# Optimization experiments

Hardware: AMD Instinct MI355X
Metric: run time of the kernel (lower is better)

The kernel has to match this reference:

```python
import jax, jax.numpy as jnp
import numpy as np

B, T, N, D, K, MP = 32, 50, 50000, 128, 16, 50
HID = (D + K) // 2  # WP_1 out features


def _normalize(x, axis=-1, eps=1e-12):
    return x / jnp.maximum(jnp.linalg.norm(x, axis=axis, keepdims=True), eps)


def _layer_norm(x, g, b, eps=1e-6):
    m = jnp.mean(x, axis=-1, keepdims=True)
    v = jnp.var(x, axis=-1, keepdims=True)
    return (x - m) * jax.lax.rsqrt(v + eps) * g + b


def setup_inputs() -> dict:
    key = jax.random.key(0)
    ks = jax.random.split(key, 20)
    std = 0.01
    session = jax.random.randint(ks[0], (B, T), 1, N + 1)  # ids >= 1, no padding
    lengths = jnp.full((B,), T, dtype=jnp.int32)
    isValidSession = jnp.ones((B * T,), dtype=bool)
    inp = {
        'session': session,
        'lengths': lengths,
        'tau': 1,
        'isValidSession': isValidSession,
        'train': 1,
        'I_emb': jax.random.normal(ks[1], (N + 1, D)) * std,
        'P_emb': jax.random.normal(ks[2], (K, D)) * std,
        'E_P_emb': jax.random.normal(ks[3], (MP, D)) * std,
        'E_S_emb': jax.random.normal(ks[4], (MP + 1, D)) * std,
        'V': _normalize(jax.random.normal(ks[5], (K, D))),
        'WP1': jax.random.normal(ks[6], (HID, D)),   # torch Linear weight [out, in]
        'WP2': jax.random.normal(ks[7], (K, HID)),
        'Wq': jax.random.normal(ks[8], (D, D)) / np.sqrt(D),
        'Wk': jax.random.normal(ks[9], (D, D)) / np.sqrt(D),
        'Wv': jax.random.normal(ks[10], (D, D)) / np.sqrt(D),
        'Wo': jax.random.normal(ks[11], (D, D)) / np.sqrt(D),
        'FF1': jax.random.normal(ks[12], (D, D)) / np.sqrt(D),
        'FF2': jax.random.normal(ks[13], (D, D)) / np.sqrt(D),
        'ln1_g': jnp.ones((D,)), 'ln1_b': jnp.zeros((D,)),
        'ln2_g': jnp.ones((D,)), 'ln2_b': jnp.zeros((D,)),
    }
    return inp


def _forward(session, lengths, tau, I_emb, P_emb, E_P_emb, E_S_emb, V,
             WP1, WP2, Wq, Wk, Wv, Wo, FF1, FF2, ln1_g, ln1_b, ln2_g, ln2_b):
    Vn = _normalize(V)                               # forward renormalizes V rows
    lf = lengths.astype(jnp.float32)
    isValidPos = (session != 0).astype(jnp.float32)  # [B,T]
    sess_emb = I_emb[session]                        # [B,T,D]
    EP = E_P_emb[jnp.arange(T) + (MP - T)]           # [T,D]
    es_idx = jnp.maximum(jnp.arange(T)[None, :] + 1 - (T - lengths[:, None]), 0)
    ES = E_S_emb[es_idx]                             # [B,T,D]

    # ---- ProxySelection (dropout in eval mode = identity) ----
    X = isValidPos[..., None] * (sess_emb + EP[None])
    X = jax.nn.leaky_relu(X @ WP1.T, 0.1) @ WP2.T    # [B,T,K]
    fP = jnp.sum(X, axis=1) / lf[:, None]
    pi = jax.nn.softmax(fP / tau, axis=-1)           # [B,K]
    p_s = pi @ P_emb                                 # [B,D]
    v = _normalize(pi @ Vn)                          # [B,D]

    # ---- SIE: single-layer self-attention encoder ----
    Xs = sess_emb + ES
    subseq = jnp.triu(jnp.ones((T, T), dtype=bool), 1)[None]        # causal
    pad = (session == 0)[:, None, :]                                # key padding
    mask = (subseq | pad)
    mask = mask.at[:, :, 0].set(False)
    non_pad = (session != 0).astype(jnp.float32)[..., None]
    q, kk, vv = Xs @ Wq.T, Xs @ Wk.T, Xs @ Wv.T
    scores = jnp.einsum('btd,bsd->bts', q, kk) / np.sqrt(D)
    scores = jnp.where(mask, -1e9, scores)
    attn = jax.nn.softmax(scores, axis=-1)
    h = (attn @ vv) @ Wo.T
    h = _layer_norm(h + Xs, ln1_g, ln1_b) * non_pad
    f = jax.nn.relu(h @ FF1.T) @ FF2.T
    s_s = _layer_norm(f + h, ln2_g, ln2_b) * non_pad                # [B,T,D]

    # project out v component per sample
    s_s_proj = s_s - v[:, None, :] * jnp.sum(v[:, None, :] * s_s, axis=-1, keepdims=True)
    orthogonal = jnp.abs(jnp.sum(v * p_s, axis=-1)) / jnp.linalg.norm(p_s, axis=-1)

    # ---- train_phase: dist(p_s+s_s_proj[b,t], I_proj_b) for all items ----
    # I_proj_b = I - v_b (v_b . I); with ||v_b||=1:
    #   ||F - I_proj||^2 = ||F||^2 - 2(F.I - (F.v)(v.I)) + ||I||^2 - (v.I)^2
    F = p_s[:, None, :] + s_s_proj                   # [B,T,D]
    vI = jnp.einsum('nd,bd->bn', I_emb, v)           # [B,N+1]
    Fv = jnp.einsum('btd,bd->bt', F, v)              # [B,T]
    FI = jnp.einsum('btd,nd->btn', F, I_emb)         # [B,T,N+1]
    Fn2 = jnp.sum(F * F, axis=-1)                    # [B,T]
    In2 = jnp.sum(I_emb * I_emb, axis=-1)[None, :] - vI * vI  # [B,N+1]
    dist = Fn2[..., None] - 2.0 * (FI - Fv[..., None] * vI[:, None, :]) + In2[:, None, :]
    return dist.reshape(B * T, N + 1), orthogonal


def reference(session, lengths, tau, isValidSession, train,
              I_emb, P_emb, E_P_emb, E_S_emb, V,
              WP1, WP2, Wq, Wk, Wv, Wo, FF1, FF2, ln1_g, ln1_b, ln2_g, ln2_b):
    # isValidSession is all-True and train=1: distance rows = all (b,t) pairs
    return _forward(session, lengths, tau, I_emb, P_emb, E_P_emb, E_S_emb, V,
                    WP1, WP2, Wq, Wk, Wv, Wo, FF1, FF2, ln1_g, ln1_b, ln2_g, ln2_b)
```

## Files before the change

kernel.cpp:

```cpp
#include <hip/hip_runtime.h>
#include <math.h>

#define B   32
#define T   50
#define N1  50001
#define D   128
#define KP  16
#define MP  50
#define HID 72
#define BT  (B*T)

typedef __attribute__((ext_vector_type(8))) short short8v;
typedef __attribute__((ext_vector_type(4))) float f32x4;

__device__ __forceinline__ unsigned short f2bf(float x) {
    unsigned u = __float_as_uint(x);
    u += 0x7fffu + ((u >> 16) & 1u);
    return (unsigned short)(u >> 16);
}

__device__ __forceinline__ float blockReduceSum128(float val, volatile float* sbuf) {
    for (int off = 32; off > 0; off >>= 1) val += __shfl_down(val, off, 64);
    __syncthreads();
    if ((threadIdx.x & 63) == 0) sbuf[threadIdx.x >> 6] = val;
    __syncthreads();
    return sbuf[0] + sbuf[1];
}

__global__ void k_proxy_x2(const int* __restrict__ session,
                           const float* __restrict__ I_emb,
                           const float* __restrict__ EP_emb,
                           const float* __restrict__ WP1,
                           const float* __restrict__ WP2,
                           float* __restrict__ X2) {
    int bt = blockIdx.x; int t = bt % T;
    int tid = threadIdx.x;
    __shared__ __align__(16) float x[D];
    __shared__ float h[HID];
    int sid = session[bt];
    float val = 0.f;
    if (sid != 0) val = I_emb[(size_t)sid * D + tid] + EP_emb[(t + MP - T) * D + tid];
    x[tid] = val;
    __syncthreads();
    if (tid < HID) {
        float acc = 0.f;
        const float4* w4 = (const float4*)(WP1 + tid * D);
        const float4* x4 = (const float4*)x;
        #pragma unroll 8
        for (int k = 0; k < D / 4; ++k) {
            float4 w = w4[k]; float4 xv = x4[k];
            acc += xv.x * w.x + xv.y * w.y + xv.z * w.z + xv.w * w.w;
        }
        h[tid] = acc > 0.f ? acc : 0.1f * acc;
    }
    __syncthreads();
    if (tid < KP) {
        float acc = 0.f;
        const float* w = WP2 + tid * HID;
        for (int k = 0; k < HID; ++k) acc += h[k] * w[k];
        X2[bt * KP + tid] = acc;
    }
}

__global__ void k_proxy_head(const float* __restrict__ X2,
                             const int* __restrict__ lengths,
                             const int* __restrict__ tau_i,
                             const float* __restrict__ P_emb,
                             const float* __restrict__ V,
                             float* __restrict__ ps_o,
                             float* __restrict__ v_o,
                             float* __restrict__ orth_o) {
    int b = blockIdx.x; int tid = threadIdx.x;
    __shared__ float pi[KP];
    __shared__ float vn[KP];
    __shared__ float sbuf[2];
    float tau = (float)tau_i[0];
    float lf = (float)lengths[b];
    if (tid < KP) {
        float s = 0.f;
        for (int t = 0; t < T; ++t) s += X2[(b * T + t) * KP + tid];
        pi[tid] = (s / lf) / tau;
    }
    if (tid < KP) {
        float s = 0.f;
        for (int d = 0; d < D; ++d) { float z = V[tid * D + d]; s += z * z; }
        vn[tid] = fmaxf(sqrtf(s), 1e-12f);
    }
    __syncthreads();
    if (tid == 0) {
        float m = pi[0];
        for (int k = 1; k < KP; ++k) m = fmaxf(m, pi[k]);
        float s = 0.f;
        for (int k = 0; k < KP; ++k) { float e = expf(pi[k] - m); pi[k] = e; s += e; }
        for (int k = 0; k < KP; ++k) pi[k] /= s;
    }
    __syncthreads();
    float p = 0.f, vt = 0.f;
    for (int k = 0; k < KP; ++k) {
        p  += pi[k] * P_emb[k * D + tid];
        vt += pi[k] * (V[k * D + tid] / vn[k]);
    }
    float vsq = blockReduceSum128(vt * vt, sbuf);
    float vv = vt / fmaxf(sqrtf(vsq), 1e-12f);
    float psq = blockReduceSum128(p * p, sbuf);
    float dvp = blockReduceSum128(vv * p, sbuf);
    ps_o[b * D + tid] = p;
    v_o[b * D + tid] = vv;
    if (tid == 0) orth_o[b] = fabsf(dvp) / sqrtf(psq);
}

__global__ void k_xs_qkv(const int* __restrict__ session,
                         const int* __restrict__ lengths,
                         const float* __restrict__ I_emb,
                         const float* __restrict__ ES_emb,
                         const float* __restrict__ Wq,
                         const float* __restrict__ Wk,
                         const float* __restrict__ Wv,
                         float* __restrict__ xs_o, float* __restrict__ q_o,
                         float* __restrict__ k_o, float* __restrict__ v_o) {
    int bt = blockIdx.x; int b = bt / T; int t = bt % T;
    int tid = threadIdx.x;
    __shared__ __align__(16) float xs[D];
    int sid = session[bt];
    int es = t + 1 - (T - lengths[b]); if (es < 0) es = 0;
    float x = I_emb[(size_t)sid * D + tid] + ES_emb[es * D + tid];
    xs[tid] = x;
    __syncthreads();
    float aq = 0.f, ak = 0.f, av = 0.f;
    const float4* wq4 = (const float4*)(Wq + tid * D);
    const float4* wk4 = (const float4*)(Wk + tid * D);
    const float4* wv4 = (const float4*)(Wv + tid * D);
    const float4* x4  = (const float4*)xs;
    #pragma unroll 8
    for (int k = 0; k < D / 4; ++k) {
        float4 xv = x4[k];
        float4 a = wq4[k], bq = wk4[k], c = wv4[k];
        aq += xv.x * a.x + xv.y * a.y + xv.z * a.z + xv.w * a.w;
        ak += xv.x * bq.x + xv.y * bq.y + xv.z * bq.z + xv.w * bq.w;
        av += xv.x * c.x + xv.y * c.y + xv.z * c.z + xv.w * c.w;
    }
    xs_o[bt * D + tid] = x; q_o[bt * D + tid] = aq; k_o[bt * D + tid] = ak; v_o[bt * D + tid] = av;
}

__global__ void k_attn(const int* __restrict__ session,
                       const float* __restrict__ q,
                       const float* __restrict__ kk,
                       const float* __restrict__ vv,
                       float* __restrict__ ho) {
    int bt = blockIdx.x; int b = bt / T; int t = bt % T;
    int tid = threadIdx.x;
    __shared__ __align__(16) float qs[D];
    __shared__ float attn[64];
    qs[tid] = q[bt * D + tid];
    __syncthreads();
    if (tid < T) {
        int s = tid;
        bool allowed = (s == 0) || ((s <= t) && (session[b * T + s] != 0));
        float sc = -1e9f;
        if (allowed) {
            float a = 0.f;
            const float4* kr = (const float4*)(kk + (size_t)(b * T + s) * D);
            const float4* q4 = (const float4*)qs;
            #pragma unroll 8
            for (int d = 0; d < D / 4; ++d) {
                float4 kv = kr[d]; float4 qv = q4[d];
                a += qv.x * kv.x + qv.y * kv.y + qv.z * kv.z + qv.w * kv.w;
            }
            sc = a * 0.088388347648318447f;
        }
        attn[s] = sc;
    }
    __syncthreads();
    if (tid < 64) {
        float vsc = (tid < T) ? attn[tid] : -1e30f;
        float m = vsc;
        for (int off = 32; off > 0; off >>= 1) m = fmaxf(m, __shfl_xor(m, off, 64));
        float e = (tid < T) ? expf(vsc - m) : 0.f;
        float ssum = e;
        for (int off = 32; off > 0; off >>= 1) ssum += __shfl_xor(ssum, off, 64);
        if (tid < T) attn[tid] = e / ssum;
    }
    __syncthreads();
    float acc = 0.f;
    for (int s = 0; s < T; ++s) acc += attn[s] * vv[(size_t)(b * T + s) * D + tid];
    ho[bt * D + tid] = acc;
}

__global__ void k_post_attn(const int* __restrict__ session,
                            const float* __restrict__ ho,
                            const float* __restrict__ Wo,
                            const float* __restrict__ xs,
                            const float* __restrict__ g1, const float* __restrict__ b1,
                            float* __restrict__ h_o) {
    int bt = blockIdx.x; int tid = threadIdx.x;
    __shared__ __align__(16) float hr[D];
    __shared__ float sbuf[2];
    hr[tid] = ho[bt * D + tid];
    __syncthreads();
    float a = 0.f;
    const float4* w4 = (const float4*)(Wo + tid * D);
    const float4* h4 = (const float4*)hr;
    #pragma unroll 8
    for (int k = 0; k < D / 4; ++k) {
        float4 w = w4[k]; float4 hv = h4[k];
        a += hv.x * w.x + hv.y * w.y + hv.z * w.z + hv.w * w.w;
    }
    float x = a + xs[bt * D + tid];
    float mean = blockReduceSum128(x, sbuf) * (1.f / D);
    float dx = x - mean;
    float var = blockReduceSum128(dx * dx, sbuf) * (1.f / D);
    float y = dx * rsqrtf(var + 1e-6f) * g1[tid] + b1[tid];
    h_o[bt * D + tid] = y * ((session[bt] != 0) ? 1.f : 0.f);
}

__global__ void k_ffn_G(const int* __restrict__ session,
                        const float* __restrict__ h,
                        const float* __restrict__ FF1, const float* __restrict__ FF2,
                        const float* __restrict__ g2, const float* __restrict__ b2,
                        const float* __restrict__ ps, const float* __restrict__ v,
                        short* __restrict__ G16, float* __restrict__ Fn2) {
    int bt = blockIdx.x; int b = bt / T; int tid = threadIdx.x;
    __shared__ __align__(16) float hr[D];
    __shared__ __align__(16) float t1[D];
    __shared__ float sbuf[2];
    float hx = h[bt * D + tid];
    hr[tid] = hx;
    __syncthreads();
    float a = 0.f;
    const float4* w14 = (const float4*)(FF1 + tid * D);
    const float4* h4 = (const float4*)hr;
    #pragma unroll 8
    for (int k = 0; k < D / 4; ++k) {
        float4 w = w14[k]; float4 hv = h4[k];
        a += hv.x * w.x + hv.y * w.y + hv.z * w.z + hv.w * w.w;
    }
    t1[tid] = fmaxf(a, 0.f);
    __syncthreads();
    float f = 0.f;
    const float4* w24 = (const float4*)(FF2 + tid * D);
    const float4* t4 = (const float4*)t1;
    #pragma unroll 8
    for (int k = 0; k < D / 4; ++k) {
        float4 w = w24[k]; float4 tv = t4[k];
        f += tv.x * w.x + tv.y * w.y + tv.z * w.z + tv.w * w.w;
    }
    float x = f + hx;
    float mean = blockReduceSum128(x, sbuf) * (1.f / D);
    float dx = x - mean;
    float var = blockReduceSum128(dx * dx, sbuf) * (1.f / D);
    float ss = dx * rsqrtf(var + 1e-6f) * g2[tid] + b2[tid];
    ss *= (session[bt] != 0) ? 1.f : 0.f;
    float vb = v[b * D + tid];
    float vs = blockReduceSum128(vb * ss, sbuf);
    float ssp = ss - vb * vs;
    float Fd = ps[b * D + tid] + ssp;
    float Fv = blockReduceSum128(Fd * vb, sbuf);
    float Gd = Fd - Fv * vb;
    float fn2 = blockReduceSum128(Fd * Fd, sbuf);
    G16[bt * D + tid] = (short)f2bf(Gd);
    if (tid == 0) Fn2[bt] = fn2;
}

#define LDK 136

__global__ __launch_bounds__(256) void k_item_mfma(const float* __restrict__ I,
                                                   const float* __restrict__ v,
                                                   float* __restrict__ In2pb) {
    __shared__ __align__(16) short Is[64][LDK];
    __shared__ __align__(16) short Vs[32][LDK];
    __shared__ float sq[64][4];
    __shared__ float in2[64];
    int n0 = blockIdx.x * 64;
    int tid = threadIdx.x;
    {
        int vr = tid >> 3;
        int vc = (tid & 7) * 16;
        const float4* src = (const float4*)&v[vr * D + vc];
        #pragma unroll
        for (int s = 0; s < 4; ++s) {
            float4 f = src[s];
            ushort4 u;
            u.x = f2bf(f.x); u.y = f2bf(f.y); u.z = f2bf(f.z); u.w = f2bf(f.w);
            *(ushort4*)&Vs[vr][vc + s * 4] = u;
        }
    }
    {
        int r = tid >> 2;
        int q = tid & 3;
        int n = n0 + r;
        float ss = 0.f;
        if (n < N1) {
            const float4* src = (const float4*)&I[(size_t)n * D + q * 32];
            #pragma unroll
            for (int s = 0; s < 8; ++s) {
                float4 f = src[s];
                ss += f.x * f.x + f.y * f.y + f.z * f.z + f.w * f.w;
                ushort4 u;
                u.x = f2bf(f.x); u.y = f2bf(f.y); u.z = f2bf(f.z); u.w = f2bf(f.w);
                *(ushort4*)&Is[r][q * 32 + s * 4] = u;
            }
        } else {
            #pragma unroll
            for (int s = 0; s < 8; ++s)
                *(ushort4*)&Is[r][q * 32 + s * 4] = make_ushort4(0, 0, 0, 0);
        }
        sq[r][q] = ss;
    }
    __syncthreads();
    if (tid < 64) in2[tid] = sq[tid][0] + sq[tid][1] + sq[tid][2] + sq[tid][3];
    __syncthreads();
    int w = tid >> 6, l = tid & 63, lr = l & 15, lg = l >> 4;
    f32x4 acc[2] = {{0.f,0.f,0.f,0.f},{0.f,0.f,0.f,0.f}};
    short8v af[4];
    #pragma unroll
    for (int ks = 0; ks < 4; ++ks)
        af[ks] = *(const short8v*)&Is[w * 16 + lr][ks * 32 + lg * 8];
    #pragma unroll
    for (int nt = 0; nt < 2; ++nt) {
        #pragma unroll
        for (int ks = 0; ks < 4; ++ks) {
            short8v bf = *(const short8v*)&Vs[nt * 16 + lr][ks * 32 + lg * 8];
            acc[nt] = __builtin_amdgcn_mfma_f32_16x16x32_bf16(af[ks], bf, acc[nt], 0, 0, 0);
        }
    }
    #pragma unroll
    for (int nt = 0; nt < 2; ++nt) {
        int b = nt * 16 + lr;
        #pragma unroll
        for (int i = 0; i < 4; ++i) {
            int item = w * 16 + lg * 4 + i;
            int n = n0 + item;
            if (n < N1) {
                float dvi = acc[nt][i];
                In2pb[(size_t)b * N1 + n] = in2[item] - dvi * dvi;
            }
        }
    }
}

__global__ __launch_bounds__(256) void k_dist_mfma(const short* __restrict__ G16,
                                                   const float* __restrict__ I,
                                                   const float* __restrict__ Fn2,
                                                   const float* __restrict__ In2pb,
                                                   float* __restrict__ out) {
    __shared__ __align__(16) short As[64][LDK];
    __shared__ __align__(16) short Bs[64][LDK];
    int bt0 = blockIdx.y * 64;
    int n0  = blockIdx.x * 64;
    int tid = threadIdx.x;
    int r = tid >> 4;
    int c = (tid & 15) * 8;
    #pragma unroll
    for (int s = 0; s < 4; ++s) {
        int row = r + s * 16;
        *(short8v*)&As[row][c] = *(const short8v*)&G16[(size_t)(bt0 + row) * D + c];
    }
    {
        int br = tid >> 2;
        int bq = (tid & 3) * 32;
        int n = n0 + br;
        if (n < N1) {
            const float4* src = (const float4*)&I[(size_t)n * D + bq];
            #pragma unroll
            for (int s = 0; s < 8; ++s) {
                float4 f = src[s];
                ushort4 u;
                u.x = f2bf(f.x); u.y = f2bf(f.y); u.z = f2bf(f.z); u.w = f2bf(f.w);
                *(ushort4*)&Bs[br][bq + s * 4] = u;
            }
        } else {
            #pragma unroll
            for (int s = 0; s < 8; ++s)
                *(ushort4*)&Bs[br][bq + s * 4] = make_ushort4(0, 0, 0, 0);
        }
    }
    __syncthreads();
    int w  = tid >> 6;
    int l  = tid & 63;
    int lr = l & 15;
    int lg = l >> 4;
    f32x4 acc[4] = {{0.f,0.f,0.f,0.f},{0.f,0.f,0.f,0.f},{0.f,0.f,0.f,0.f},{0.f,0.f,0.f,0.f}};
    short8v af[4];
    #pragma unroll
    for (int ks = 0; ks < 4; ++ks)
        af[ks] = *(const short8v*)&As[w * 16 + lr][ks * 32 + lg * 8];
    #pragma unroll
    for (int nt = 0; nt < 4; ++nt) {
        #pragma unroll
        for (int ks = 0; ks < 4; ++ks) {
            short8v bf = *(const short8v*)&Bs[nt * 16 + lr][ks * 32 + lg * 8];
            acc[nt] = __builtin_amdgcn_mfma_f32_16x16x32_bf16(af[ks], bf, acc[nt], 0, 0, 0);
        }
    }
    #pragma unroll
    for (int nt = 0; nt < 4; ++nt) {
        int col = n0 + nt * 16 + lr;
        if (col < N1) {
            #pragma unroll
            for (int i = 0; i < 4; ++i) {
                int row = bt0 + w * 16 + lg * 4 + i;
                int b = row / T;
                out[(size_t)row * N1 + col] = Fn2[row] + In2pb[(size_t)b * N1 + col] - 2.f * acc[nt][i];
            }
        }
    }
}

extern "C" void kernel_launch(void* const* d_in, const int* in_sizes, int n_in,
                              void* d_out, int out_size, void* d_ws, size_t ws_size,
                              hipStream_t stream) {
    const int*   session = (const int*)d_in[0];
    const int*   lengths = (const int*)d_in[1];
    const int*   tau     = (const int*)d_in[2];
    const float* I_emb   = (const float*)d_in[5];
    const float* P_emb   = (const float*)d_in[6];
    const float* EP      = (const float*)d_in[7];
    const float* ES      = (const float*)d_in[8];
    const float* V       = (const float*)d_in[9];
    const float* WP1     = (const float*)d_in[10];
    const float* WP2     = (const float*)d_in[11];
    const float* Wq      = (const float*)d_in[12];
    const float* Wk      = (const float*)d_in[13];
    const float* Wv      = (const float*)d_in[14];
    const float* Wo      = (const float*)d_in[15];
    const float* FF1     = (const float*)d_in[16];
    const float* FF2     = (const float*)d_in[17];
    const float* g1      = (const float*)d_in[18];
    const float* b1      = (const float*)d_in[19];
    const float* g2      = (const float*)d_in[20];
    const float* b2      = (const float*)d_in[21];
    float* out = (float*)d_out;
    float* ws  = (float*)d_ws;

    float* wsX2   = ws;
    float* wsPs   = wsX2 + 25600;
    float* wsV    = wsPs + 4096;
    float* wsXs   = wsV + 4096;
    float* wsQ    = wsXs + 204800;
    float* wsK    = wsQ + 204800;
    float* wsVv   = wsK + 204800;
    float* wsHo   = wsVv + 204800;
    float* wsH    = wsHo + 204800;
    float* wsFn2  = wsH + 204800;
    float* wsIn2  = wsFn2 + 1600;
    short* wsG16  = (short*)(wsIn2 + 1600032);

    float* orth_out = out + (size_t)BT * N1;

    k_proxy_x2 <<<BT, 128, 0, stream>>>(session, I_emb, EP, WP1, WP2, wsX2);
    k_proxy_head<<<B, 128, 0, stream>>>(wsX2, lengths, tau, P_emb, V, wsPs, wsV, orth_out);
    k_xs_qkv  <<<BT, 128, 0, stream>>>(session, lengths, I_emb, ES, Wq, Wk, Wv,
                                       wsXs, wsQ, wsK, wsVv);
    k_attn    <<<BT, 128, 0, stream>>>(session, wsQ, wsK, wsVv, wsHo);
    k_post_attn<<<BT, 128, 0, stream>>>(session, wsHo, Wo, wsXs, g1, b1, wsH);
    k_ffn_G   <<<BT, 128, 0, stream>>>(session, wsH, FF1, FF2, g2, b2, wsPs, wsV,
                                       wsG16, wsFn2);
    k_item_mfma<<<(N1 + 63) / 64, 256, 0, stream>>>(I_emb, wsV, wsIn2);
    dim3 gdist((N1 + 63) / 64, BT / 64);
    k_dist_mfma<<<gdist, 256, 0, stream>>>(wsG16, I_emb, wsFn2, wsIn2, out);
}
```

Before: 308.3 us.

## Fuse front-end kernels, cache bf16 item table, enlarge distance GEMM tile

Merges the proxy and QKV kernels into one, and merges attention, post-attention layernorm and the FFN into one kernel, which removes launches and intermediate global round trips. The item-norm kernel now also writes a bf16 copy of the item embeddings. The distance kernel reads that copy instead of re-converting fp32 rows in every block, and each block now covers 128 session rows, so item tiles are reloaded fewer times. The cost is extra workspace and an extra bf16 write pass over the item table, plus higher register and LDS use per distance block.

```diff
diff --git a/kernel.cpp b/kernel.cpp
--- a/kernel.cpp
+++ b/kernel.cpp
@@ -27,21 +27,47 @@
     return sbuf[0] + sbuf[1];
 }
 
-__global__ void k_proxy_x2(const int* __restrict__ session,
-                           const float* __restrict__ I_emb,
-                           const float* __restrict__ EP_emb,
-                           const float* __restrict__ WP1,
-                           const float* __restrict__ WP2,
-                           float* __restrict__ X2) {
-    int bt = blockIdx.x; int t = bt % T;
+__global__ void k_fused_emb(const int* __restrict__ session,
+                            const int* __restrict__ lengths,
+                            const float* __restrict__ I_emb,
+                            const float* __restrict__ EP_emb,
+                            const float* __restrict__ ES_emb,
+                            const float* __restrict__ WP1,
+                            const float* __restrict__ WP2,
+                            const float* __restrict__ Wq,
+                            const float* __restrict__ Wk,
+                            const float* __restrict__ Wv,
+                            float* __restrict__ X2,
+                            float* __restrict__ xs_o, float* __restrict__ q_o,
+                            float* __restrict__ k_o, float* __restrict__ v_o) {
+    int bt = blockIdx.x; int b = bt / T; int t = bt % T;
     int tid = threadIdx.x;
     __shared__ __align__(16) float x[D];
+    __shared__ __align__(16) float xs[D];
     __shared__ float h[HID];
     int sid = session[bt];
-    float val = 0.f;
-    if (sid != 0) val = I_emb[(size_t)sid * D + tid] + EP_emb[(t + MP - T) * D + tid];
-    x[tid] = val;
-    __syncthreads();
+    float ie = I_emb[(size_t)sid * D + tid];
+    float xv_ = (sid != 0) ? (ie + EP_emb[(t + MP - T) * D + tid]) : 0.f;
+    int es = t + 1 - (T - lengths[b]); if (es < 0) es = 0;
+    float xsv = ie + ES_emb[es * D + tid];
+    x[tid] = xv_;
+    xs[tid] = xsv;
+    __syncthreads();
+    float aq = 0.f, ak = 0.f, av = 0.f;
+    {
+        const float4* wq4 = (const float4*)(Wq + tid * D);
+        const float4* wk4 = (const float4*)(Wk + tid * D);
+        const float4* wv4 = (const float4*)(Wv + tid * D);
+        const float4* x4  = (const float4*)xs;
+        #pragma unroll 8
+        for (int k = 0; k < D / 4; ++k) {
+            float4 xv = x4[k];
+            float4 a = wq4[k], bq = wk4[k], c = wv4[k];
+            aq += xv.x * a.x + xv.y * a.y + xv.z * a.z + xv.w * a.w;
+            ak += xv.x * bq.x + xv.y * bq.y + xv.z * bq.z + xv.w * bq.w;
+            av += xv.x * c.x + xv.y * c.y + xv.z * c.z + xv.w * c.w;
+        }
+    }
     if (tid < HID) {
         float acc = 0.f;
         const float4* w4 = (const float4*)(WP1 + tid * D);
@@ -53,6 +79,8 @@
         }
         h[tid] = acc > 0.f ? acc : 0.1f * acc;
     }
+    xs_o[bt * D + tid] = xsv;
+    q_o[bt * D + tid] = aq; k_o[bt * D + tid] = ak; v_o[bt * D + tid] = av;
     __syncthreads();
     if (tid < KP) {
         float acc = 0.f;
@@ -109,48 +137,24 @@
     if (tid == 0) orth_o[b] = fabsf(dvp) / sqrtf(psq);
 }
 
-__global__ void k_xs_qkv(const int* __restrict__ session,
-                         const int* __restrict__ lengths,
-                         const float* __restrict__ I_emb,
-                         const float* __restrict__ ES_emb,
-                         const float* __restrict__ Wq,
-                         const float* __restrict__ Wk,
-                         const float* __restrict__ Wv,
-                         float* __restrict__ xs_o, float* __restrict__ q_o,
-                         float* __restrict__ k_o, float* __restrict__ v_o) {
-    int bt = blockIdx.x; int b = bt / T; int t = bt % T;
-    int tid = threadIdx.x;
-    __shared__ __align__(16) float xs[D];
-    int sid = session[bt];
-    int es = t + 1 - (T - lengths[b]); if (es < 0) es = 0;
-    float x = I_emb[(size_t)sid * D + tid] + ES_emb[es * D + tid];
-    xs[tid] = x;
-    __syncthreads();
-    float aq = 0.f, ak = 0.f, av = 0.f;
-    const float4* wq4 = (const float4*)(Wq + tid * D);
-    const float4* wk4 = (const float4*)(Wk + tid * D);
-    const float4* wv4 = (const float4*)(Wv + tid * D);
-    const float4* x4  = (const float4*)xs;
-    #pragma unroll 8
-    for (int k = 0; k < D / 4; ++k) {
-        float4 xv = x4[k];
-        float4 a = wq4[k], bq = wk4[k], c = wv4[k];
-        aq += xv.x * a.x + xv.y * a.y + xv.z * a.z + xv.w * a.w;
-        ak += xv.x * bq.x + xv.y * bq.y + xv.z * bq.z + xv.w * bq.w;
-        av += xv.x * c.x + xv.y * c.y + xv.z * c.z + xv.w * c.w;
-    }
-    xs_o[bt * D + tid] = x; q_o[bt * D + tid] = aq; k_o[bt * D + tid] = ak; v_o[bt * D + tid] = av;
-}
-
-__global__ void k_attn(const int* __restrict__ session,
-                       const float* __restrict__ q,
-                       const float* __restrict__ kk,
-                       const float* __restrict__ vv,
-                       float* __restrict__ ho) {
+__global__ void k_fused_attn(const int* __restrict__ session,
+                             const float* __restrict__ q,
+                             const float* __restrict__ kk,
+                             const float* __restrict__ vv,
+                             const float* __restrict__ xs,
+                             const float* __restrict__ Wo,
+                             const float* __restrict__ g1, const float* __restrict__ b1,
+                             const float* __restrict__ FF1, const float* __restrict__ FF2,
+                             const float* __restrict__ g2, const float* __restrict__ b2,
+                             const float* __restrict__ ps, const float* __restrict__ v,
+                             short* __restrict__ G16, float* __restrict__ Fn2) {
     int bt = blockIdx.x; int b = bt / T; int t = bt % T;
     int tid = threadIdx.x;
     __shared__ __align__(16) float qs[D];
+    __shared__ __align__(16) float buf1[D];
+    __shared__ __align__(16) float buf2[D];
     __shared__ float attn[64];
+    __shared__ float sbuf[2];
     qs[tid] = q[bt * D + tid];
     __syncthreads();
     if (tid < T) {
@@ -183,72 +187,53 @@
     __syncthreads();
     float acc = 0.f;
     for (int s = 0; s < T; ++s) acc += attn[s] * vv[(size_t)(b * T + s) * D + tid];
-    ho[bt * D + tid] = acc;
-}
-
-__global__ void k_post_attn(const int* __restrict__ session,
-                            const float* __restrict__ ho,
-                            const float* __restrict__ Wo,
-                            const float* __restrict__ xs,
-                            const float* __restrict__ g1, const float* __restrict__ b1,
-                            float* __restrict__ h_o) {
-    int bt = blockIdx.x; int tid = threadIdx.x;
-    __shared__ __align__(16) float hr[D];
-    __shared__ float sbuf[2];
-    hr[tid] = ho[bt * D + tid];
+    buf1[tid] = acc;
     __syncthreads();
     float a = 0.f;
-    const float4* w4 = (const float4*)(Wo + tid * D);
-    const float4* h4 = (const float4*)hr;
-    #pragma unroll 8
-    for (int k = 0; k < D / 4; ++k) {
-        float4 w = w4[k]; float4 hv = h4[k];
-        a += hv.x * w.x + hv.y * w.y + hv.z * w.z + hv.w * w.w;
-    }
-    float x = a + xs[bt * D + tid];
-    float mean = blockReduceSum128(x, sbuf) * (1.f / D);
-    float dx = x - mean;
+    {
+        const float4* w4 = (const float4*)(Wo + tid * D);
+        const float4* h4 = (const float4*)buf1;
+        #pragma unroll 8
+        for (int k = 0; k < D / 4; ++k) {
+            float4 w = w4[k]; float4 hv = h4[k];
+            a += hv.x * w.x + hv.y * w.y + hv.z * w.z + hv.w * w.w;
+        }
+    }
+    float x1 = a + xs[bt * D + tid];
+    float mean = blockReduceSum128(x1, sbuf) * (1.f / D);
+    float dx = x1 - mean;
     float var = blockReduceSum128(dx * dx, sbuf) * (1.f / D);
-    float y = dx * rsqrtf(var + 1e-6f) * g1[tid] + b1[tid];
-    h_o[bt * D + tid] = y * ((session[bt] != 0) ? 1.f : 0.f);
-}
-
-__global__ void k_ffn_G(const int* __restrict__ session,
-                        const float* __restrict__ h,
-                        const float* __restrict__ FF1, const float* __restrict__ FF2,
-                        const float* __restrict__ g2, const float* __restrict__ b2,
-                        const float* __restrict__ ps, const float* __restrict__ v,
-                        short* __restrict__ G16, float* __restrict__ Fn2) {
-    int bt = blockIdx.x; int b = bt / T; int tid = threadIdx.x;
-    __shared__ __align__(16) float hr[D];
-    __shared__ __align__(16) float t1[D];
-    __shared__ float sbuf[2];
-    float hx = h[bt * D + tid];
-    hr[tid] = hx;
-    __syncthreads();
-    float a = 0.f;
-    const float4* w14 = (const float4*)(FF1 + tid * D);
-    const float4* h4 = (const float4*)hr;
-    #pragma unroll 8
-    for (int k = 0; k < D / 4; ++k) {
-        float4 w = w14[k]; float4 hv = h4[k];
-        a += hv.x * w.x + hv.y * w.y + hv.z * w.z + hv.w * w.w;
-    }
-    t1[tid] = fmaxf(a, 0.f);
+    float hx = (dx * rsqrtf(var + 1e-6f) * g1[tid] + b1[tid]) * ((session[bt] != 0) ? 1.f : 0.f);
+    buf2[tid] = hx;
+    __syncthreads();
+    float a1 = 0.f;
+    {
+        const float4* w4 = (const float4*)(FF1 + tid * D);
+        const float4* h4 = (const float4*)buf2;
+        #pragma unroll 8
+        for (int k = 0; k < D / 4; ++k) {
+            float4 w = w4[k]; float4 hv = h4[k];
+            a1 += hv.x * w.x + hv.y * w.y + hv.z * w.z + hv.w * w.w;
+        }
+    }
+    __syncthreads();
+    buf1[tid] = fmaxf(a1, 0.f);
     __syncthreads();
     float f = 0.f;
-    const float4* w24 = (const float4*)(FF2 + tid * D);
-    const float4* t4 = (const float4*)t1;
-    #pragma unroll 8
-    for (int k = 0; k < D / 4; ++k) {
-        float4 w = w24[k]; float4 tv = t4[k];
-        f += tv.x * w.x + tv.y * w.y + tv.z * w.z + tv.w * w.w;
-    }
-    float x = f + hx;
-    float mean = blockReduceSum128(x, sbuf) * (1.f / D);
-    float dx = x - mean;
-    float var = blockReduceSum128(dx * dx, sbuf) * (1.f / D);
-    float ss = dx * rsqrtf(var + 1e-6f) * g2[tid] + b2[tid];
+    {
+        const float4* w4 = (const float4*)(FF2 + tid * D);
+        const float4* t4 = (const float4*)buf1;
+        #pragma unroll 8
+        for (int k = 0; k < D / 4; ++k) {
+            float4 w = w4[k]; float4 tv = t4[k];
+            f += tv.x * w.x + tv.y * w.y + tv.z * w.z + tv.w * w.w;
+        }
+    }
+    float x2 = f + hx;
+    float mean2 = blockReduceSum128(x2, sbuf) * (1.f / D);
+    float dx2 = x2 - mean2;
+    float var2 = blockReduceSum128(dx2 * dx2, sbuf) * (1.f / D);
+    float ss = dx2 * rsqrtf(var2 + 1e-6f) * g2[tid] + b2[tid];
     ss *= (session[bt] != 0) ? 1.f : 0.f;
     float vb = v[b * D + tid];
     float vs = blockReduceSum128(vb * ss, sbuf);
@@ -265,7 +250,8 @@
 
 __global__ __launch_bounds__(256) void k_item_mfma(const float* __restrict__ I,
                                                    const float* __restrict__ v,
-                                                   float* __restrict__ In2pb) {
+                                                   float* __restrict__ In2pb,
+                                                   unsigned short* __restrict__ I16) {
     __shared__ __align__(16) short Is[64][LDK];
     __shared__ __align__(16) short Vs[32][LDK];
     __shared__ float sq[64][4];
@@ -286,25 +272,26 @@
     }
     {
         int r = tid >> 2;
-        int q = tid & 3;
+        int qq = tid & 3;
         int n = n0 + r;
         float ss = 0.f;
         if (n < N1) {
-            const float4* src = (const float4*)&I[(size_t)n * D + q * 32];
+            const float4* src = (const float4*)&I[(size_t)n * D + qq * 32];
             #pragma unroll
             for (int s = 0; s < 8; ++s) {
                 float4 f = src[s];
                 ss += f.x * f.x + f.y * f.y + f.z * f.z + f.w * f.w;
                 ushort4 u;
                 u.x = f2bf(f.x); u.y = f2bf(f.y); u.z = f2bf(f.z); u.w = f2bf(f.w);
-                *(ushort4*)&Is[r][q * 32 + s * 4] = u;
+                *(ushort4*)&Is[r][qq * 32 + s * 4] = u;
+                *(ushort4*)&I16[(size_t)n * D + qq * 32 + s * 4] = u;
             }
         } else {
             #pragma unroll
             for (int s = 0; s < 8; ++s)
-                *(ushort4*)&Is[r][q * 32 + s * 4] = make_ushort4(0, 0, 0, 0);
-        }
-        sq[r][q] = ss;
+                *(ushort4*)&Is[r][qq * 32 + s * 4] = make_ushort4(0, 0, 0, 0);
+        }
+        sq[r][qq] = ss;
     }
     __syncthreads();
     if (tid < 64) in2[tid] = sq[tid][0] + sq[tid][1] + sq[tid][2] + sq[tid][3];
@@ -339,68 +326,77 @@
 }
 
 __global__ __launch_bounds__(256) void k_dist_mfma(const short* __restrict__ G16,
-                                                   const float* __restrict__ I,
+                                                   const unsigned short* __restrict__ I16,
                                                    const float* __restrict__ Fn2,
                                                    const float* __restrict__ In2pb,
                                                    float* __restrict__ out) {
-    __shared__ __align__(16) short As[64][LDK];
+    __shared__ __align__(16) short As[128][LDK];
     __shared__ __align__(16) short Bs[64][LDK];
-    int bt0 = blockIdx.y * 64;
     int n0  = blockIdx.x * 64;
+    int bt0 = blockIdx.y * 128;
     int tid = threadIdx.x;
     int r = tid >> 4;
     int c = (tid & 15) * 8;
     #pragma unroll
+    for (int s = 0; s < 8; ++s) {
+        int row = r + s * 16;
+        short8v gv = {};
+        if (bt0 + row < BT) gv = *(const short8v*)&G16[(size_t)(bt0 + row) * D + c];
+        *(short8v*)&As[row][c] = gv;
+    }
+    #pragma unroll
     for (int s = 0; s < 4; ++s) {
         int row = r + s * 16;
-        *(short8v*)&As[row][c] = *(const short8v*)&G16[(size_t)(bt0 + row) * D + c];
-    }
-    {
-        int br = tid >> 2;
-        int bq = (tid & 3) * 32;
-        int n = n0 + br;
-        if (n < N1) {
-            const float4* src = (const float4*)&I[(size_t)n * D + bq];
-            #pragma unroll
-            for (int s = 0; s < 8; ++s) {
-                float4 f = src[s];
-                ushort4 u;
-                u.x = f2bf(f.x); u.y = f2bf(f.y); u.z = f2bf(f.z); u.w = f2bf(f.w);
-                *(ushort4*)&Bs[br][bq + s * 4] = u;
-            }
-        } else {
-            #pragma unroll
-            for (int s = 0; s < 8; ++s)
-                *(ushort4*)&Bs[br][bq + s * 4] = make_ushort4(0, 0, 0, 0);
-        }
+        int n = n0 + row;
+        short8v bv = {};
+        if (n < N1) bv = *(const short8v*)&I16[(size_t)n * D + c];
+        *(short8v*)&Bs[row][c] = bv;
     }
     __syncthreads();
     int w  = tid >> 6;
     int l  = tid & 63;
     int lr = l & 15;
     int lg = l >> 4;
-    f32x4 acc[4] = {{0.f,0.f,0.f,0.f},{0.f,0.f,0.f,0.f},{0.f,0.f,0.f,0.f},{0.f,0.f,0.f,0.f}};
-    short8v af[4];
-    #pragma unroll
-    for (int ks = 0; ks < 4; ++ks)
-        af[ks] = *(const short8v*)&As[w * 16 + lr][ks * 32 + lg * 8];
+    short8v af[2][4];
+    #pragma unroll
+    for (int mi = 0; mi < 2; ++mi)
+        #pragma unroll
+        for (int ks = 0; ks < 4; ++ks)
+            af[mi][ks] = *(const short8v*)&As[w * 32 + mi * 16 + lr][ks * 32 + lg * 8];
+    f32x4 acc[2][4];
+    #pragma unroll
+    for (int mi = 0; mi < 2; ++mi)
+        #pragma unroll
+        for (int nt = 0; nt < 4; ++nt) acc[mi][nt] = (f32x4){0.f, 0.f, 0.f, 0.f};
     #pragma unroll
     for (int nt = 0; nt < 4; ++nt) {
-        #pragma unroll
-        for (int ks = 0; ks < 4; ++ks) {
-            short8v bf = *(const short8v*)&Bs[nt * 16 + lr][ks * 32 + lg * 8];
-            acc[nt] = __builtin_amdgcn_mfma_f32_16x16x32_bf16(af[ks], bf, acc[nt], 0, 0, 0);
-        }
-    }
-    #pragma unroll
-    for (int nt = 0; nt < 4; ++nt) {
-        int col = n0 + nt * 16 + lr;
-        if (col < N1) {
+        short8v bf[4];
+        #pragma unroll
+        for (int ks = 0; ks < 4; ++ks)
+            bf[ks] = *(const short8v*)&Bs[nt * 16 + lr][ks * 32 + lg * 8];
+        #pragma unroll
+        for (int mi = 0; mi < 2; ++mi)
+            #pragma unroll
+            for (int ks = 0; ks < 4; ++ks)
+                acc[mi][nt] = __builtin_amdgcn_mfma_f32_16x16x32_bf16(af[mi][ks], bf[ks], acc[mi][nt], 0, 0, 0);
+    }
+    #pragma unroll
+    for (int mi = 0; mi < 2; ++mi) {
+        int rb = bt0 + w * 32 + mi * 16 + lg * 4;
+        if (rb < BT) {
+            float4 fn4 = *(const float4*)&Fn2[rb];
+            float fnv[4] = {fn4.x, fn4.y, fn4.z, fn4.w};
             #pragma unroll
             for (int i = 0; i < 4; ++i) {
-                int row = bt0 + w * 16 + lg * 4 + i;
+                int row = rb + i;
                 int b = row / T;
-                out[(size_t)row * N1 + col] = Fn2[row] + In2pb[(size_t)b * N1 + col] - 2.f * acc[nt][i];
+                const float* inrow = In2pb + (size_t)b * N1;
+                float* orow = out + (size_t)row * N1;
+                #pragma unroll
+                for (int nt = 0; nt < 4; ++nt) {
+                    int col = n0 + nt * 16 + lr;
+                    if (col < N1) orow[col] = fnv[i] + inrow[col] - 2.f * acc[mi][nt][i];
+                }
             }
         }
     }
@@ -439,23 +435,21 @@
     float* wsQ    = wsXs + 204800;
     float* wsK    = wsQ + 204800;
     float* wsVv   = wsK + 204800;
-    float* wsHo   = wsVv + 204800;
-    float* wsH    = wsHo + 204800;
-    float* wsFn2  = wsH + 204800;
+    float* wsFn2  = wsVv + 204800;
     float* wsIn2  = wsFn2 + 1600;
     short* wsG16  = (short*)(wsIn2 + 1600032);
+    unsigned short* wsI16 = (unsigned short*)(wsG16 + 204800);
 
     float* orth_out = out + (size_t)BT * N1;
 
-    k_proxy_x2 <<<BT, 128, 0, stream>>>(session, I_emb, EP, WP1, WP2, wsX2);
+    k_fused_emb <<<BT, 128, 0, stream>>>(session, lengths, I_emb, EP, ES,
+                                         WP1, WP2, Wq, Wk, Wv,
+                                         wsX2, wsXs, wsQ, wsK, wsVv);
     k_proxy_head<<<B, 128, 0, stream>>>(wsX2, lengths, tau, P_emb, V, wsPs, wsV, orth_out);
-    k_xs_qkv  <<<BT, 128, 0, stream>>>(session, lengths, I_emb, ES, Wq, Wk, Wv,
-                                       wsXs, wsQ, wsK, wsVv);
-    k_attn    <<<BT, 128, 0, stream>>>(session, wsQ, wsK, wsVv, wsHo);
-    k_post_attn<<<BT, 128, 0, stream>>>(session, wsHo, Wo, wsXs, g1, b1, wsH);
-    k_ffn_G   <<<BT, 128, 0, stream>>>(session, wsH, FF1, FF2, g2, b2, wsPs, wsV,
-                                       wsG16, wsFn2);
-    k_item_mfma<<<(N1 + 63) / 64, 256, 0, stream>>>(I_emb, wsV, wsIn2);
-    dim3 gdist((N1 + 63) / 64, BT / 64);
-    k_dist_mfma<<<gdist, 256, 0, stream>>>(wsG16, I_emb, wsFn2, wsIn2, out);
-}
+    k_fused_attn<<<BT, 128, 0, stream>>>(session, wsQ, wsK, wsVv, wsXs,
+                                         Wo, g1, b1, FF1, FF2, g2, b2,
+                                         wsPs, wsV, wsG16, wsFn2);
+    k_item_mfma <<<(N1 + 63) / 64, 256, 0, stream>>>(I_emb, wsV, wsIn2, wsI16);
+    dim3 gdist((N1 + 63) / 64, (BT + 127) / 128);
+    k_dist_mfma <<<gdist, 256, 0, stream>>>(wsG16, wsI16, wsFn2, wsIn2, out);
+}
```

Result: no change. 308.5 us (+0.1%).
